# Kernel tuning notes

Measured on AMD Instinct MI355X. Metric: run time of the kernel, lower is better.

Reference implementation:

```python
import jax, jax.numpy as jnp
import numpy as np

N_NODES = 50000
N_EDGES = 800000
NODE_DIM = 64
EDGE_DIM = 32


def _glorot(key, shape):
    fan_in, fan_out = shape
    lim = (6.0 / (fan_in + fan_out)) ** 0.5
    return jax.random.uniform(key, shape, jnp.float32, -lim, lim)


def setup_inputs() -> dict:
    key = jax.random.key(0)
    ks = jax.random.split(key, 12)
    x = jax.random.normal(ks[0], (N_NODES, NODE_DIM), jnp.float32)
    edge_index = jax.random.randint(ks[1], (2, N_EDGES), 0, N_NODES, jnp.int64)
    edge_attr = jax.random.normal(ks[2], (N_EDGES, EDGE_DIM), jnp.float32)
    # edge_mlp: Linear(edge_dim + 2*node_dim -> node_dim), ReLU, Linear(node_dim -> node_dim)
    W1e = _glorot(ks[3], (EDGE_DIM + 2 * NODE_DIM, NODE_DIM))
    b1e = jnp.zeros((NODE_DIM,), jnp.float32)
    W2e = _glorot(ks[4], (NODE_DIM, NODE_DIM))
    b2e = jnp.zeros((NODE_DIM,), jnp.float32)
    # node_mlp: Linear(2*node_dim -> node_dim), ReLU, Linear(node_dim -> node_dim)
    W1n = _glorot(ks[5], (2 * NODE_DIM, NODE_DIM))
    b1n = jnp.zeros((NODE_DIM,), jnp.float32)
    W2n = _glorot(ks[6], (NODE_DIM, NODE_DIM))
    b2n = jnp.zeros((NODE_DIM,), jnp.float32)
    return {"x": x, "edge_index": edge_index, "edge_attr": edge_attr,
            "W1e": W1e, "b1e": b1e, "W2e": W2e, "b2e": b2e,
            "W1n": W1n, "b1n": b1n, "W2n": W2n, "b2n": b2n}


def reference(x, edge_index, edge_attr, W1e, b1e, W2e, b2e, W1n, b1n, W2n, b2n):
    row, col = edge_index[0], edge_index[1]
    # gather endpoint features: [E, node_dim] each
    edge_input = jnp.concatenate([x[row], x[col], edge_attr], axis=-1)  # [E, 2D+De]
    h = jax.nn.relu(edge_input @ W1e + b1e)
    edge_output = h @ W2e + b2e  # [E, D]
    # scatter-add into target nodes
    aggregated = jnp.zeros_like(x).at[col].add(edge_output)  # [N, D]
    node_input = jnp.concatenate([x, aggregated], axis=-1)  # [N, 2D]
    g = jax.nn.relu(node_input @ W1n + b1n)
    node_output = g @ W2n + b2n
    return jax.nn.relu(node_output + x)
```

## Files before the change

kernel.cpp:

```cpp
#include <hip/hip_runtime.h>

typedef float    f32x4 __attribute__((ext_vector_type(4)));
typedef short    s16x8 __attribute__((ext_vector_type(8)));
typedef unsigned u32x2 __attribute__((ext_vector_type(2)));

#define ND   64
#define DE   32
#define K1   160
#define K1P  168
#define K2P  72
#define KN   128
#define KNP  136

__device__ __forceinline__ ushort f2bf(float f) {
  unsigned u = __float_as_uint(f);
  return (ushort)((u + 0x7fffu + ((u >> 16) & 1u)) >> 16);
}
__device__ __forceinline__ float relu_f(float v) { return v > 0.f ? v : 0.f; }
__device__ __forceinline__ unsigned cvtpk(float lo, float hi) {
  unsigned r;
  asm("v_cvt_pk_bf16_f32 %0, %1, %2" : "=v"(r) : "v"(lo), "v"(hi));
  return r;
}

__launch_bounds__(256, 3)
__global__ void gc_edge(const float* __restrict__ x,
                        const int* __restrict__ eidx,
                        const float* __restrict__ eattr,
                        const float* __restrict__ W1e, const float* __restrict__ b1e,
                        ushort* __restrict__ hsum,
                        float* __restrict__ deg,
                        int E, int ngroups) {
  __shared__ ushort   w1t[ND][K1P];
  __shared__ ushort   strip[4][16][K1P];
  __shared__ unsigned hb[4][16][33];

  const int t    = threadIdx.x;
  const int lane = t & 63;
  const int w    = t >> 6;
  const int l15  = lane & 15;
  const int lhi  = lane >> 4;
  const int k8   = lhi * 8;

  for (int i = t; i < K1 * ND; i += 256) w1t[i & 63][i >> 6] = f2bf(W1e[i]);
  __syncthreads();

  float bias[4];
  #pragma unroll
  for (int n = 0; n < 4; ++n) bias[n] = b1e[n * 16 + l15];

  const int el   = lane >> 2;
  const int part = lane & 3;
  const int wid  = blockIdx.x * 4 + w;
  const int nw   = gridDim.x * 4;

  for (int g = wid; g < ngroups; g += nw) {
    const int e0 = g * 16;
    int myidx = 0;
    if (lane < 32)
      myidx = (lane < 16) ? eidx[e0 + lane] : eidx[E + e0 + (lane - 16)];

    const int rrow = __shfl(myidx, el);
    const int rcol = __shfl(myidx, 16 + el);
    const float* xr = x + (size_t)rrow * ND + part * 4;
    const float* xc = x + (size_t)rcol * ND + part * 4;
    const float* ap = eattr + ((size_t)e0 + (lane >> 3)) * DE + (lane & 7) * 4;

    f32x4 vr[4], vc[4], va[2];
    #pragma unroll
    for (int i = 0; i < 4; ++i) vr[i] = *(const f32x4*)(xr + i * 16);
    #pragma unroll
    for (int i = 0; i < 4; ++i) vc[i] = *(const f32x4*)(xc + i * 16);
    va[0] = *(const f32x4*)ap;
    va[1] = *(const f32x4*)(ap + 8 * DE);

    #pragma unroll
    for (int i = 0; i < 4; ++i) {
      u32x2 d = { cvtpk(vr[i].x, vr[i].y), cvtpk(vr[i].z, vr[i].w) };
      *(u32x2*)&strip[w][el][i * 16 + part * 4] = d;
    }
    #pragma unroll
    for (int i = 0; i < 4; ++i) {
      u32x2 d = { cvtpk(vc[i].x, vc[i].y), cvtpk(vc[i].z, vc[i].w) };
      *(u32x2*)&strip[w][el][64 + i * 16 + part * 4] = d;
    }
    #pragma unroll
    for (int i = 0; i < 2; ++i) {
      u32x2 d = { cvtpk(va[i].x, va[i].y), cvtpk(va[i].z, va[i].w) };
      *(u32x2*)&strip[w][(lane >> 3) + i * 8][128 + (lane & 7) * 4] = d;
    }
    asm volatile("s_waitcnt lgkmcnt(0)" ::: "memory");

    f32x4 acc[4] = {};
    #pragma unroll
    for (int ks = 0; ks < 5; ++ks) {
      s16x8 a = *(const s16x8*)&strip[w][l15][ks * 32 + k8];
      #pragma unroll
      for (int n = 0; n < 4; ++n) {
        s16x8 b = *(const s16x8*)&w1t[n * 16 + l15][ks * 32 + k8];
        acc[n] = __builtin_amdgcn_mfma_f32_16x16x32_bf16(a, b, acc[n], 0, 0, 0);
      }
    }

    if (lane >= 16 && lane < 32) atomicAdd(&deg[myidx], 1.0f);

    #pragma unroll
    for (int n = 0; n < 4; ++n) {
      #pragma unroll
      for (int j = 0; j < 4; ++j) {
        float r = relu_f(acc[n][j] + bias[n]);
        float p = __shfl_xor(r, 1);
        if (!(l15 & 1)) hb[w][lhi * 4 + j][(n * 16 + l15) >> 1] = cvtpk(r, p);
      }
    }
    asm volatile("s_waitcnt lgkmcnt(0)" ::: "memory");

    #pragma unroll
    for (int i = 0; i < 8; ++i) {
      int ee = (lane >> 4) + (i >> 1) * 4;
      int q  = (lane & 15) + (i & 1) * 16;
      int sc = __shfl(myidx, 16 + ee);
      uint64_t ad = (uint64_t)((unsigned*)hsum + (size_t)sc * 32 + q);
      unsigned data = hb[w][ee][q];
      asm volatile("global_atomic_pk_add_bf16 %0, %1, off" :: "v"(ad), "v"(data) : "memory");
    }
  }
}

__launch_bounds__(256, 2)
__global__ void gc_node(const float* __restrict__ x,
                        const ushort* __restrict__ hsum,
                        const float* __restrict__ deg,
                        const float* __restrict__ W2e, const float* __restrict__ b2e,
                        const float* __restrict__ W1n, const float* __restrict__ b1n,
                        const float* __restrict__ W2n, const float* __restrict__ b2n,
                        float* __restrict__ out, int N) {
  __shared__ ushort w2et[ND][K2P];
  __shared__ ushort w1nt[ND][KNP];
  __shared__ ushort w2nt[ND][K2P];
  __shared__ ushort in_lds[64][KNP];
  __shared__ ushort h_lds[64][K2P];

  const int t    = threadIdx.x;
  const int lane = t & 63;
  const int w    = t >> 6;
  const int l15  = lane & 15;
  const int lhi  = lane >> 4;
  const int k8   = lhi * 8;

  for (int i = t; i < 64 * ND; i += 256) w2et[i & 63][i >> 6] = f2bf(W2e[i]);
  for (int i = t; i < KN * ND; i += 256) w1nt[i & 63][i >> 6] = f2bf(W1n[i]);
  for (int i = t; i < 64 * ND; i += 256) w2nt[i & 63][i >> 6] = f2bf(W2n[i]);

  const int n0 = blockIdx.x * 64;
  #pragma unroll
  for (int i = 0; i < 4; ++i) {
    int chunk = t + i * 256;
    int r = chunk >> 4, p = chunk & 15;
    int node = n0 + r; if (node >= N) node = N - 1;
    f32x4 v = *(const f32x4*)(x + (size_t)node * ND + p * 4);
    unsigned* dst = (unsigned*)&in_lds[r][p * 4];
    dst[0] = cvtpk(v.x, v.y); dst[1] = cvtpk(v.z, v.w);
  }

  const int strip = w * 16;
  {
    int arow = strip + l15;
    int node = n0 + arow; if (node >= N) node = N - 1;
    const s16x8* ph = (const s16x8*)(hsum + (size_t)node * ND);
    s16x8 a0 = ph[lhi];
    s16x8 a1 = ph[4 + lhi];
    __syncthreads();
    f32x4 accg[4] = {};
    #pragma unroll
    for (int n = 0; n < 4; ++n) {
      s16x8 b0 = *(const s16x8*)&w2et[n * 16 + l15][k8];
      s16x8 b1 = *(const s16x8*)&w2et[n * 16 + l15][32 + k8];
      accg[n] = __builtin_amdgcn_mfma_f32_16x16x32_bf16(a0, b0, accg[n], 0, 0, 0);
      accg[n] = __builtin_amdgcn_mfma_f32_16x16x32_bf16(a1, b1, accg[n], 0, 0, 0);
    }
    #pragma unroll
    for (int n = 0; n < 4; ++n) {
      int d = n * 16 + l15;
      float b2 = b2e[d];
      #pragma unroll
      for (int j = 0; j < 4; ++j) {
        int r = strip + lhi * 4 + j;
        int node2 = n0 + r; if (node2 >= N) node2 = N - 1;
        float ag = accg[n][j] + deg[node2] * b2;
        in_lds[r][64 + d] = f2bf(ag);
      }
    }
  }
  __syncthreads();

  const int ar = strip + l15;
  f32x4 acc1[4] = {};
  #pragma unroll
  for (int ks = 0; ks < 4; ++ks) {
    s16x8 a = *(const s16x8*)&in_lds[ar][ks * 32 + k8];
    #pragma unroll
    for (int n = 0; n < 4; ++n) {
      s16x8 b = *(const s16x8*)&w1nt[n * 16 + l15][ks * 32 + k8];
      acc1[n] = __builtin_amdgcn_mfma_f32_16x16x32_bf16(a, b, acc1[n], 0, 0, 0);
    }
  }
  #pragma unroll
  for (int n = 0; n < 4; ++n) {
    int d = n * 16 + l15;
    float bias = b1n[d];
    #pragma unroll
    for (int j = 0; j < 4; ++j)
      h_lds[strip + lhi * 4 + j][d] = f2bf(relu_f(acc1[n][j] + bias));
  }
  __syncthreads();

  f32x4 acc2[4] = {};
  #pragma unroll
  for (int ks = 0; ks < 2; ++ks) {
    s16x8 a = *(const s16x8*)&h_lds[ar][ks * 32 + k8];
    #pragma unroll
    for (int n = 0; n < 4; ++n) {
      s16x8 b = *(const s16x8*)&w2nt[n * 16 + l15][ks * 32 + k8];
      acc2[n] = __builtin_amdgcn_mfma_f32_16x16x32_bf16(a, b, acc2[n], 0, 0, 0);
    }
  }
  #pragma unroll
  for (int n = 0; n < 4; ++n) {
    int d = n * 16 + l15;
    float bias = b2n[d];
    #pragma unroll
    for (int j = 0; j < 4; ++j) {
      int node = n0 + strip + lhi * 4 + j;
      if (node < N) {
        float xv = x[(size_t)node * ND + d];
        out[(size_t)node * ND + d] = relu_f(acc2[n][j] + bias + xv);
      }
    }
  }
}

extern "C" void kernel_launch(void* const* d_in, const int* in_sizes, int n_in,
                              void* d_out, int out_size, void* d_ws, size_t ws_size,
                              hipStream_t stream) {
  const float* x     = (const float*)d_in[0];
  const int*   eidx  = (const int*)d_in[1];
  const float* eattr = (const float*)d_in[2];
  const float* W1e   = (const float*)d_in[3];
  const float* b1e   = (const float*)d_in[4];
  const float* W2e   = (const float*)d_in[5];
  const float* b2e   = (const float*)d_in[6];
  const float* W1n   = (const float*)d_in[7];
  const float* b1n   = (const float*)d_in[8];
  const float* W2n   = (const float*)d_in[9];
  const float* b2n   = (const float*)d_in[10];
  float* out = (float*)d_out;

  const int N = in_sizes[0] / ND;
  const int E = in_sizes[1] / 2;
  const int ngroups = E / 16;

  ushort* hsum = (ushort*)d_ws;
  float*  degp = (float*)(hsum + (size_t)N * ND);

  hipMemsetAsync(d_ws, 0, (size_t)N * ND * 2 + (size_t)N * 4, stream);

  gc_edge<<<2048, 256, 0, stream>>>(x, eidx, eattr, W1e, b1e, hsum, degp, E, ngroups);

  int grid_n = (N + 63) / 64;
  gc_node<<<grid_n, 256, 0, stream>>>(x, hsum, degp, W2e, b2e, W1n, b1n, W2n, b2n, out, N);
}
```

Measured before the change: 167.7 us.

## Bucket edges by destination node to replace global atomics with LDS accumulation

Adds a counting-sort preprocessing pipeline (histogram, prefix scan, placement) that groups edges into 32-node buckets by destination, so each block handles one bucket. The destination node features come from an LDS window and the per-edge results accumulate in LDS with shared atomics before one bf16 store per node. This aims to remove the global bf16 scatter atomics and the repeated gathers of destination rows. In exchange it adds three extra launches, a single-block serial scan, an extra global pass over the edges with global atomics, and possible load imbalance across buckets. The old atomic path is kept as a fallback when the workspace is too small.

```diff
diff --git a/kernel.cpp b/kernel.cpp
--- a/kernel.cpp
+++ b/kernel.cpp
@@ -8,9 +8,13 @@
 #define DE   32
 #define K1   160
 #define K1P  168
+#define SP   104
+#define XWP  72
 #define K2P  72
 #define KN   128
 #define KNP  136
+#define BKT  32
+#define EMASK 0x1FFFFFF
 
 __device__ __forceinline__ ushort f2bf(float f) {
   unsigned u = __float_as_uint(f);
@@ -23,17 +27,66 @@
   return r;
 }
 
+__global__ void gc_hist(const int* __restrict__ eidx, float* __restrict__ deg, int E) {
+  int i = blockIdx.x * blockDim.x + threadIdx.x;
+  for (; i < E; i += gridDim.x * blockDim.x)
+    atomicAdd(&deg[eidx[E + i]], 1.0f);
+}
+
+__global__ void gc_prefix(const float* __restrict__ deg, int N, int NB,
+                          int* __restrict__ offset, int* __restrict__ cursor) {
+  __shared__ int cnt[2048];
+  const int t = threadIdx.x;
+  for (int b = t; b < NB; b += 256) {
+    int s = 0, base = b * BKT;
+    #pragma unroll
+    for (int j = 0; j < BKT; ++j) {
+      int node = base + j;
+      s += (node < N) ? (int)deg[node] : 0;
+    }
+    cnt[b] = s;
+  }
+  __syncthreads();
+  if (t < 64) {
+    int running = 0;
+    for (int base = 0; base < NB; base += 64) {
+      int b = base + t;
+      int v = (b < NB) ? cnt[b] : 0;
+      int incl = v;
+      #pragma unroll
+      for (int d = 1; d < 64; d <<= 1) {
+        int u = __shfl_up(incl, d);
+        if (t >= d) incl += u;
+      }
+      if (b < NB) { int ex = running + incl - v; offset[b] = ex; cursor[b] = ex; }
+      running += __shfl(incl, 63);
+    }
+    if (t == 0) offset[NB] = running;
+  }
+}
+
+__global__ void gc_place(const int* __restrict__ eidx, int* __restrict__ cursor,
+                         int2* __restrict__ recs, int E) {
+  int i = blockIdx.x * blockDim.x + threadIdx.x;
+  for (; i < E; i += gridDim.x * blockDim.x) {
+    int col = eidx[E + i];
+    int row = eidx[i];
+    int b = col >> 5;
+    int pos = atomicAdd(&cursor[b], 1);
+    recs[pos] = make_int2(row, ((col & 31) << 25) | i);
+  }
+}
+
 __launch_bounds__(256, 3)
-__global__ void gc_edge(const float* __restrict__ x,
-                        const int* __restrict__ eidx,
-                        const float* __restrict__ eattr,
-                        const float* __restrict__ W1e, const float* __restrict__ b1e,
-                        ushort* __restrict__ hsum,
-                        float* __restrict__ deg,
-                        int E, int ngroups) {
-  __shared__ ushort   w1t[ND][K1P];
-  __shared__ ushort   strip[4][16][K1P];
-  __shared__ unsigned hb[4][16][33];
+__global__ void gc_edge_b(const float* __restrict__ x,
+                          const float* __restrict__ eattr,
+                          const float* __restrict__ W1e, const float* __restrict__ b1e,
+                          const int2* __restrict__ recs, const int* __restrict__ offset,
+                          ushort* __restrict__ hsum, int N) {
+  __shared__ ushort w1t[ND][K1P];
+  __shared__ ushort strip[4][16][SP];
+  __shared__ ushort xwin[BKT][XWP];
+  __shared__ float  acc[BKT][ND];
 
   const int t    = threadIdx.x;
   const int lane = t & 63;
@@ -41,18 +94,138 @@
   const int l15  = lane & 15;
   const int lhi  = lane >> 4;
   const int k8   = lhi * 8;
+  const int bkt  = blockIdx.x;
+  const int node0 = bkt * BKT;
 
   for (int i = t; i < K1 * ND; i += 256) w1t[i & 63][i >> 6] = f2bf(W1e[i]);
+  #pragma unroll
+  for (int i = 0; i < 2; ++i) {
+    int c = t + i * 256;
+    int r = c >> 4, p = c & 15;
+    int node = node0 + r;
+    f32x4 v = {0.f, 0.f, 0.f, 0.f};
+    if (node < N) v = *(const f32x4*)(x + (size_t)node * ND + p * 4);
+    u32x2 d = { cvtpk(v.x, v.y), cvtpk(v.z, v.w) };
+    *(u32x2*)&xwin[r][p * 4] = d;
+  }
+  #pragma unroll
+  for (int i = 0; i < 8; ++i) {
+    int c = t + i * 256;
+    acc[c >> 6][c & 63] = 0.f;
+  }
   __syncthreads();
 
   float bias[4];
   #pragma unroll
   for (int n = 0; n < 4; ++n) bias[n] = b1e[n * 16 + l15];
 
-  const int el   = lane >> 2;
-  const int part = lane & 3;
-  const int wid  = blockIdx.x * 4 + w;
-  const int nw   = gridDim.x * 4;
+  const int start = offset[bkt], end = offset[bkt + 1];
+  const int nIter = (end - start + 63) >> 6;
+  const int el = lane >> 2, part = lane & 3;
+
+  for (int it = 0; it < nIter; ++it) {
+    const int eBase = start + it * 64 + w * 16;
+    int recx = 0, recy = 0;
+    if (lane < 16) {
+      int idx = eBase + lane;
+      if (idx >= end) idx = end - 1;
+      int2 r_ = recs[idx];
+      recx = r_.x; recy = r_.y;
+    }
+    const int rowv  = __shfl(recx, el);
+    const int eidA  = __shfl(recy, lane >> 3) & EMASK;
+    const int eidB  = __shfl(recy, 8 + (lane >> 3)) & EMASK;
+    const int myloc = __shfl(recy, l15) >> 25;
+
+    const float* xr = x + (size_t)rowv * ND + part * 4;
+    f32x4 vr[4];
+    #pragma unroll
+    for (int i = 0; i < 4; ++i) vr[i] = *(const f32x4*)(xr + i * 16);
+    f32x4 va0 = *(const f32x4*)(eattr + (size_t)eidA * DE + (lane & 7) * 4);
+    f32x4 va1 = *(const f32x4*)(eattr + (size_t)eidB * DE + (lane & 7) * 4);
+
+    #pragma unroll
+    for (int i = 0; i < 4; ++i) {
+      u32x2 d = { cvtpk(vr[i].x, vr[i].y), cvtpk(vr[i].z, vr[i].w) };
+      *(u32x2*)&strip[w][el][i * 16 + part * 4] = d;
+    }
+    { u32x2 d = { cvtpk(va0.x, va0.y), cvtpk(va0.z, va0.w) };
+      *(u32x2*)&strip[w][lane >> 3][64 + (lane & 7) * 4] = d; }
+    { u32x2 d = { cvtpk(va1.x, va1.y), cvtpk(va1.z, va1.w) };
+      *(u32x2*)&strip[w][8 + (lane >> 3)][64 + (lane & 7) * 4] = d; }
+    asm volatile("s_waitcnt lgkmcnt(0)" ::: "memory");
+
+    s16x8 a0 = *(const s16x8*)&strip[w][l15][k8];
+    s16x8 a1 = *(const s16x8*)&strip[w][l15][32 + k8];
+    s16x8 a2 = *(const s16x8*)&xwin[myloc][k8];
+    s16x8 a3 = *(const s16x8*)&xwin[myloc][32 + k8];
+    s16x8 a4 = *(const s16x8*)&strip[w][l15][64 + k8];
+
+    f32x4 accv[4] = {};
+    #pragma unroll
+    for (int n = 0; n < 4; ++n) {
+      const ushort* wr = &w1t[n * 16 + l15][0];
+      accv[n] = __builtin_amdgcn_mfma_f32_16x16x32_bf16(a0, *(const s16x8*)&wr[k8],        accv[n], 0, 0, 0);
+      accv[n] = __builtin_amdgcn_mfma_f32_16x16x32_bf16(a1, *(const s16x8*)&wr[32 + k8],   accv[n], 0, 0, 0);
+      accv[n] = __builtin_amdgcn_mfma_f32_16x16x32_bf16(a2, *(const s16x8*)&wr[64 + k8],   accv[n], 0, 0, 0);
+      accv[n] = __builtin_amdgcn_mfma_f32_16x16x32_bf16(a3, *(const s16x8*)&wr[96 + k8],   accv[n], 0, 0, 0);
+      accv[n] = __builtin_amdgcn_mfma_f32_16x16x32_bf16(a4, *(const s16x8*)&wr[128 + k8],  accv[n], 0, 0, 0);
+    }
+
+    #pragma unroll
+    for (int j = 0; j < 4; ++j) {
+      const int  locj  = __shfl(recy, lhi * 4 + j) >> 25;
+      const bool valid = (eBase + lhi * 4 + j) < end;
+      if (valid) {
+        #pragma unroll
+        for (int n = 0; n < 4; ++n)
+          atomicAdd(&acc[locj][n * 16 + l15], relu_f(accv[n][j] + bias[n]));
+      }
+    }
+  }
+  __syncthreads();
+
+  #pragma unroll
+  for (int i = 0; i < 2; ++i) {
+    int c = t + i * 256;
+    int r = c >> 4, p = (c & 15) * 4;
+    int node = node0 + r;
+    if (node < N) {
+      f32x4 v = *(const f32x4*)&acc[r][p];
+      u32x2 d = { cvtpk(v.x, v.y), cvtpk(v.z, v.w) };
+      *(u32x2*)&hsum[(size_t)node * ND + p] = d;
+    }
+  }
+}
+
+__launch_bounds__(256, 3)
+__global__ void gc_edge_atomic(const float* __restrict__ x,
+                               const int* __restrict__ eidx,
+                               const float* __restrict__ eattr,
+                               const float* __restrict__ W1e, const float* __restrict__ b1e,
+                               ushort* __restrict__ hsum, float* __restrict__ deg,
+                               int E, int ngroups) {
+  __shared__ ushort   w1t[ND][K1P];
+  __shared__ ushort   strip[4][16][K1P];
+  __shared__ unsigned hb[4][16][33];
+
+  const int t    = threadIdx.x;
+  const int lane = t & 63;
+  const int w    = t >> 6;
+  const int l15  = lane & 15;
+  const int lhi  = lane >> 4;
+  const int k8   = lhi * 8;
+
+  for (int i = t; i < K1 * ND; i += 256) w1t[i & 63][i >> 6] = f2bf(W1e[i]);
+  __syncthreads();
+
+  float bias[4];
+  #pragma unroll
+  for (int n = 0; n < 4; ++n) bias[n] = b1e[n * 16 + l15];
+
+  const int el = lane >> 2, part = lane & 3;
+  const int wid = blockIdx.x * 4 + w;
+  const int nw  = gridDim.x * 4;
 
   for (int g = wid; g < ngroups; g += nw) {
     const int e0 = g * 16;
@@ -256,17 +429,30 @@
   const float* b2n   = (const float*)d_in[10];
   float* out = (float*)d_out;
 
-  const int N = in_sizes[0] / ND;
-  const int E = in_sizes[1] / 2;
-  const int ngroups = E / 16;
-
-  ushort* hsum = (ushort*)d_ws;
-  float*  degp = (float*)(hsum + (size_t)N * ND);
-
-  hipMemsetAsync(d_ws, 0, (size_t)N * ND * 2 + (size_t)N * 4, stream);
-
-  gc_edge<<<2048, 256, 0, stream>>>(x, eidx, eattr, W1e, b1e, hsum, degp, E, ngroups);
+  const int N  = in_sizes[0] / ND;
+  const int E  = in_sizes[1] / 2;
+  const int NB = (N + BKT - 1) / BKT;
+
+  char* ws = (char*)d_ws;
+  ushort* hsum   = (ushort*)ws;
+  float*  deg    = (float*)(ws + (size_t)N * ND * 2);
+  size_t  off    = (size_t)N * ND * 2 + (size_t)N * 4;
+  int2*   recs   = (int2*)(ws + off);
+  int*    offset = (int*)(ws + off + (size_t)E * 8);
+  int*    cursor = offset + (NB + 1);
+  size_t  need   = off + (size_t)E * 8 + (size_t)(2 * NB + 1) * 4;
+
+  if (ws_size >= need) {
+    hipMemsetAsync(deg, 0, (size_t)N * 4, stream);
+    gc_hist<<<1024, 256, 0, stream>>>(eidx, deg, E);
+    gc_prefix<<<1, 256, 0, stream>>>(deg, N, NB, offset, cursor);
+    gc_place<<<1024, 256, 0, stream>>>(eidx, cursor, recs, E);
+    gc_edge_b<<<NB, 256, 0, stream>>>(x, eattr, W1e, b1e, recs, offset, hsum, N);
+  } else {
+    hipMemsetAsync(d_ws, 0, (size_t)N * ND * 2 + (size_t)N * 4, stream);
+    gc_edge_atomic<<<2048, 256, 0, stream>>>(x, eidx, eattr, W1e, b1e, hsum, deg, E, E / 16);
+  }
 
   int grid_n = (N + 63) / 64;
-  gc_node<<<grid_n, 256, 0, stream>>>(x, hsum, degp, W2e, b2e, W1n, b1n, W2n, b2n, out, N);
-}
+  gc_node<<<grid_n, 256, 0, stream>>>(x, hsum, deg, W2e, b2e, W1n, b1n, W2n, b2n, out, N);
+}
```

Result: slower. 566.6 us (+237.9%).

## Replace atomic scatter-add with CSR sort and per-node gather aggregation

Applied to the files above, without the earlier changes.

The edge kernel now writes each edge's hidden activation to a per-edge bf16 buffer instead of atomically adding into node sums. A single-block prefix scan over the degree counts and an atomic placement pass then build a CSR list of edges grouped by target node. A gather kernel sums each node's incoming edges without atomics. W1 fragments are also preloaded into registers. This trades the contended bf16 atomics for extra kernels, a serial single-block scan, and a large per-edge intermediate buffer. If the workspace is too small, the code falls back to the old atomic path.

```diff
diff --git a/kernel.cpp b/kernel.cpp
--- a/kernel.cpp
+++ b/kernel.cpp
@@ -3,6 +3,7 @@
 typedef float    f32x4 __attribute__((ext_vector_type(4)));
 typedef short    s16x8 __attribute__((ext_vector_type(8)));
 typedef unsigned u32x2 __attribute__((ext_vector_type(2)));
+typedef unsigned u32x4 __attribute__((ext_vector_type(4)));
 
 #define ND   64
 #define DE   32
@@ -16,6 +17,7 @@
   unsigned u = __float_as_uint(f);
   return (ushort)((u + 0x7fffu + ((u >> 16) & 1u)) >> 16);
 }
+__device__ __forceinline__ float bf2f(unsigned u) { return __uint_as_float(u << 16); }
 __device__ __forceinline__ float relu_f(float v) { return v > 0.f ? v : 0.f; }
 __device__ __forceinline__ unsigned cvtpk(float lo, float hi) {
   unsigned r;
@@ -24,16 +26,16 @@
 }
 
 __launch_bounds__(256, 3)
-__global__ void gc_edge(const float* __restrict__ x,
-                        const int* __restrict__ eidx,
-                        const float* __restrict__ eattr,
-                        const float* __restrict__ W1e, const float* __restrict__ b1e,
-                        ushort* __restrict__ hsum,
-                        float* __restrict__ deg,
-                        int E, int ngroups) {
+__global__ void gc_edge_h(const float* __restrict__ x,
+                          const int* __restrict__ eidx,
+                          const float* __restrict__ eattr,
+                          const float* __restrict__ W1e, const float* __restrict__ b1e,
+                          ushort* __restrict__ hbuf,
+                          float* __restrict__ deg,
+                          int E, int ngroups) {
   __shared__ ushort   w1t[ND][K1P];
   __shared__ ushort   strip[4][16][K1P];
-  __shared__ unsigned hb[4][16][33];
+  __shared__ unsigned hb[4][16][36];
 
   const int t    = threadIdx.x;
   const int lane = t & 63;
@@ -45,14 +47,193 @@
   for (int i = t; i < K1 * ND; i += 256) w1t[i & 63][i >> 6] = f2bf(W1e[i]);
   __syncthreads();
 
+  s16x8 bf[4][5];
+  #pragma unroll
+  for (int n = 0; n < 4; ++n)
+    #pragma unroll
+    for (int ks = 0; ks < 5; ++ks)
+      bf[n][ks] = *(const s16x8*)&w1t[n * 16 + l15][ks * 32 + k8];
+
   float bias[4];
   #pragma unroll
   for (int n = 0; n < 4; ++n) bias[n] = b1e[n * 16 + l15];
 
-  const int el   = lane >> 2;
-  const int part = lane & 3;
-  const int wid  = blockIdx.x * 4 + w;
-  const int nw   = gridDim.x * 4;
+  const int el = lane >> 2, part = lane & 3;
+  const int wid = blockIdx.x * 4 + w;
+  const int nw  = gridDim.x * 4;
+
+  for (int g = wid; g < ngroups; g += nw) {
+    const int e0 = g * 16;
+    int myidx = 0;
+    if (lane < 32)
+      myidx = (lane < 16) ? eidx[e0 + lane] : eidx[E + e0 + (lane - 16)];
+
+    const int rrow = __shfl(myidx, el);
+    const int rcol = __shfl(myidx, 16 + el);
+    const float* xr = x + (size_t)rrow * ND + part * 4;
+    const float* xc = x + (size_t)rcol * ND + part * 4;
+    const float* ap = eattr + ((size_t)e0 + (lane >> 3)) * DE + (lane & 7) * 4;
+
+    f32x4 vr[4], vc[4], va[2];
+    #pragma unroll
+    for (int i = 0; i < 4; ++i) vr[i] = *(const f32x4*)(xr + i * 16);
+    #pragma unroll
+    for (int i = 0; i < 4; ++i) vc[i] = *(const f32x4*)(xc + i * 16);
+    va[0] = *(const f32x4*)ap;
+    va[1] = *(const f32x4*)(ap + 8 * DE);
+
+    #pragma unroll
+    for (int i = 0; i < 4; ++i) {
+      u32x2 d = { cvtpk(vr[i].x, vr[i].y), cvtpk(vr[i].z, vr[i].w) };
+      *(u32x2*)&strip[w][el][i * 16 + part * 4] = d;
+    }
+    #pragma unroll
+    for (int i = 0; i < 4; ++i) {
+      u32x2 d = { cvtpk(vc[i].x, vc[i].y), cvtpk(vc[i].z, vc[i].w) };
+      *(u32x2*)&strip[w][el][64 + i * 16 + part * 4] = d;
+    }
+    #pragma unroll
+    for (int i = 0; i < 2; ++i) {
+      u32x2 d = { cvtpk(va[i].x, va[i].y), cvtpk(va[i].z, va[i].w) };
+      *(u32x2*)&strip[w][(lane >> 3) + i * 8][128 + (lane & 7) * 4] = d;
+    }
+    asm volatile("s_waitcnt lgkmcnt(0)" ::: "memory");
+
+    f32x4 acc[4] = {};
+    #pragma unroll
+    for (int ks = 0; ks < 5; ++ks) {
+      s16x8 a = *(const s16x8*)&strip[w][l15][ks * 32 + k8];
+      #pragma unroll
+      for (int n = 0; n < 4; ++n)
+        acc[n] = __builtin_amdgcn_mfma_f32_16x16x32_bf16(a, bf[n][ks], acc[n], 0, 0, 0);
+    }
+
+    if (lane >= 16 && lane < 32) atomicAdd(&deg[myidx], 1.0f);
+
+    #pragma unroll
+    for (int n = 0; n < 4; ++n) {
+      #pragma unroll
+      for (int j = 0; j < 4; ++j) {
+        float r = relu_f(acc[n][j] + bias[n]);
+        float p = __shfl_xor(r, 1);
+        if (!(l15 & 1)) hb[w][lhi * 4 + j][(n * 16 + l15) >> 1] = cvtpk(r, p);
+      }
+    }
+    asm volatile("s_waitcnt lgkmcnt(0)" ::: "memory");
+
+    unsigned* hrow = (unsigned*)hbuf + (size_t)(e0 + (lane >> 2)) * 32 + (lane & 3) * 4;
+    u32x4 d0 = *(const u32x4*)&hb[w][lane >> 2][(lane & 3) * 4];
+    u32x4 d1 = *(const u32x4*)&hb[w][lane >> 2][(lane & 3) * 4 + 16];
+    *(u32x4*)hrow = d0;
+    *(u32x4*)(hrow + 16) = d1;
+  }
+}
+
+__global__ void gc_prefix(const float* __restrict__ deg, int N,
+                          int* __restrict__ offset, int* __restrict__ cursor) {
+  __shared__ int wt[16], we[16];
+  __shared__ int srun, ctot;
+  const int t = threadIdx.x, lane = t & 63, w = t >> 6;
+  if (t == 0) srun = 0;
+  __syncthreads();
+  for (int base = 0; base < N; base += 1024) {
+    int i = base + t;
+    int v = (i < N) ? (int)deg[i] : 0;
+    int incl = v;
+    #pragma unroll
+    for (int d = 1; d < 64; d <<= 1) {
+      int u = __shfl_up(incl, d);
+      if (lane >= d) incl += u;
+    }
+    if (lane == 63) wt[w] = incl;
+    __syncthreads();
+    if (t == 0) {
+      int run = 0;
+      #pragma unroll
+      for (int k = 0; k < 16; ++k) { we[k] = run; run += wt[k]; }
+      ctot = run;
+    }
+    __syncthreads();
+    if (i < N) {
+      int ex = srun + we[w] + incl - v;
+      offset[i] = ex; cursor[i] = ex;
+    }
+    __syncthreads();
+    if (t == 0) srun += ctot;
+    __syncthreads();
+  }
+  if (t == 0) offset[N] = srun;
+}
+
+__global__ void gc_place(const int* __restrict__ eidx, int* __restrict__ cursor,
+                         int* __restrict__ recs, int E) {
+  int i = blockIdx.x * blockDim.x + threadIdx.x;
+  for (; i < E; i += gridDim.x * blockDim.x) {
+    int col = eidx[E + i];
+    int pos = atomicAdd(&cursor[col], 1);
+    recs[pos] = i;
+  }
+}
+
+__launch_bounds__(256, 8)
+__global__ void gc_agg(const ushort* __restrict__ hbuf,
+                       const int* __restrict__ recs,
+                       const int* __restrict__ offset,
+                       ushort* __restrict__ hsum, int N) {
+  const int t = threadIdx.x, lane = t & 63, w = t >> 6;
+  const int v = blockIdx.x * 4 + w;
+  if (v >= N) return;
+  const int g = lane >> 4, l15 = lane & 15;
+  const int start = offset[v], end = offset[v + 1];
+
+  float a0 = 0.f, a1 = 0.f, a2 = 0.f, a3 = 0.f;
+  for (int c = start; c < end; c += 4) {
+    int idx = c + g;
+    if (idx < end) {
+      int eid = recs[idx];
+      u32x2 d = *(const u32x2*)(hbuf + (size_t)eid * ND + l15 * 4);
+      a0 += bf2f(d.x & 0xffffu); a1 += bf2f(d.x >> 16);
+      a2 += bf2f(d.y & 0xffffu); a3 += bf2f(d.y >> 16);
+    }
+  }
+  a0 += __shfl_xor(a0, 16); a1 += __shfl_xor(a1, 16);
+  a2 += __shfl_xor(a2, 16); a3 += __shfl_xor(a3, 16);
+  a0 += __shfl_xor(a0, 32); a1 += __shfl_xor(a1, 32);
+  a2 += __shfl_xor(a2, 32); a3 += __shfl_xor(a3, 32);
+  if (lane < 16) {
+    u32x2 o = { cvtpk(a0, a1), cvtpk(a2, a3) };
+    *(u32x2*)&hsum[(size_t)v * ND + l15 * 4] = o;
+  }
+}
+
+__launch_bounds__(256, 3)
+__global__ void gc_edge_atomic(const float* __restrict__ x,
+                               const int* __restrict__ eidx,
+                               const float* __restrict__ eattr,
+                               const float* __restrict__ W1e, const float* __restrict__ b1e,
+                               ushort* __restrict__ hsum, float* __restrict__ deg,
+                               int E, int ngroups) {
+  __shared__ ushort   w1t[ND][K1P];
+  __shared__ ushort   strip[4][16][K1P];
+  __shared__ unsigned hb[4][16][33];
+
+  const int t    = threadIdx.x;
+  const int lane = t & 63;
+  const int w    = t >> 6;
+  const int l15  = lane & 15;
+  const int lhi  = lane >> 4;
+  const int k8   = lhi * 8;
+
+  for (int i = t; i < K1 * ND; i += 256) w1t[i & 63][i >> 6] = f2bf(W1e[i]);
+  __syncthreads();
+
+  float bias[4];
+  #pragma unroll
+  for (int n = 0; n < 4; ++n) bias[n] = b1e[n * 16 + l15];
+
+  const int el = lane >> 2, part = lane & 3;
+  const int wid = blockIdx.x * 4 + w;
+  const int nw  = gridDim.x * 4;
 
   for (int g = wid; g < ngroups; g += nw) {
     const int e0 = g * 16;
@@ -258,15 +439,29 @@
 
   const int N = in_sizes[0] / ND;
   const int E = in_sizes[1] / 2;
-  const int ngroups = E / 16;
-
-  ushort* hsum = (ushort*)d_ws;
-  float*  degp = (float*)(hsum + (size_t)N * ND);
-
-  hipMemsetAsync(d_ws, 0, (size_t)N * ND * 2 + (size_t)N * 4, stream);
-
-  gc_edge<<<2048, 256, 0, stream>>>(x, eidx, eattr, W1e, b1e, hsum, degp, E, ngroups);
-
-  int grid_n = (N + 63) / 64;
-  gc_node<<<grid_n, 256, 0, stream>>>(x, hsum, degp, W2e, b2e, W1n, b1n, W2n, b2n, out, N);
-}
+
+  char* ws = (char*)d_ws;
+  ushort* hbuf   = (ushort*)ws;
+  ushort* hsum   = (ushort*)(ws + (size_t)E * ND * 2);
+  float*  deg    = (float*)(ws + (size_t)E * ND * 2 + (size_t)N * ND * 2);
+  int*    offset = (int*)((char*)deg + (size_t)N * 4);
+  int*    cursor = offset + (N + 1);
+  int*    recs   = cursor + N;
+  size_t need = (size_t)E * ND * 2 + (size_t)N * ND * 2 + (size_t)N * 4
+              + (size_t)(2 * N + 1) * 4 + (size_t)E * 4;
+
+  if (ws_size >= need) {
+    hipMemsetAsync(deg, 0, (size_t)N * 4, stream);
+    gc_edge_h<<<2048, 256, 0, stream>>>(x, eidx, eattr, W1e, b1e, hbuf, deg, E, E / 16);
+    gc_prefix<<<1, 1024, 0, stream>>>(deg, N, offset, cursor);
+    gc_place<<<1024, 256, 0, stream>>>(eidx, cursor, recs, E);
+    gc_agg<<<(N + 3) / 4, 256, 0, stream>>>(hbuf, recs, offset, hsum, N);
+    gc_node<<<(N + 63) / 64, 256, 0, stream>>>(x, hsum, deg, W2e, b2e, W1n, b1n, W2n, b2n, out, N);
+  } else {
+    ushort* hsum_fb = (ushort*)ws;
+    float*  deg_fb  = (float*)(ws + (size_t)N * ND * 2);
+    hipMemsetAsync(ws, 0, (size_t)N * ND * 2 + (size_t)N * 4, stream);
+    gc_edge_atomic<<<2048, 256, 0, stream>>>(x, eidx, eattr, W1e, b1e, hsum_fb, deg_fb, E, E / 16);
+    gc_node<<<(N + 63) / 64, 256, 0, stream>>>(x, hsum_fb, deg_fb, W2e, b2e, W1n, b1n, W2n, b2n, out, N);
+  }
+}
```

Result: slower. 253.0 us (+50.9%).

## Precompute per-node projections of x through W1e and gather them per edge

Applied to the files above, without the earlier changes.

The first edge-MLP layer is split algebraically into x[row]@W1a + x[col]@W1b + attr@W1c. A new kernel computes both node projections once per node into a bf16 PQ buffer. The edge kernel then gathers 64-dim bf16 projections instead of 128 fp32 features, runs only the 32-wide attribute MFMA, adds the three parts and applies ReLU before the atomic scatter. This cuts per-edge gather bytes and MFMA work, at the cost of an extra kernel, an extra workspace buffer, and bf16 rounding of the intermediate projections.

```diff
diff --git a/kernel.cpp b/kernel.cpp
--- a/kernel.cpp
+++ b/kernel.cpp
@@ -3,14 +3,14 @@
 typedef float    f32x4 __attribute__((ext_vector_type(4)));
 typedef short    s16x8 __attribute__((ext_vector_type(8)));
 typedef unsigned u32x2 __attribute__((ext_vector_type(2)));
+typedef unsigned u32x4 __attribute__((ext_vector_type(4)));
 
 #define ND   64
 #define DE   32
-#define K1   160
-#define K1P  168
-#define K2P  72
 #define KN   128
 #define KNP  136
+#define K2P  72
+#define WBP  40
 
 __device__ __forceinline__ ushort f2bf(float f) {
   unsigned u = __float_as_uint(f);
@@ -22,37 +22,101 @@
   asm("v_cvt_pk_bf16_f32 %0, %1, %2" : "=v"(r) : "v"(lo), "v"(hi));
   return r;
 }
-
-__launch_bounds__(256, 3)
-__global__ void gc_edge(const float* __restrict__ x,
-                        const int* __restrict__ eidx,
-                        const float* __restrict__ eattr,
-                        const float* __restrict__ W1e, const float* __restrict__ b1e,
-                        ushort* __restrict__ hsum,
-                        float* __restrict__ deg,
-                        int E, int ngroups) {
-  __shared__ ushort   w1t[ND][K1P];
-  __shared__ ushort   strip[4][16][K1P];
-  __shared__ unsigned hb[4][16][33];
-
-  const int t    = threadIdx.x;
-  const int lane = t & 63;
-  const int w    = t >> 6;
-  const int l15  = lane & 15;
-  const int lhi  = lane >> 4;
-  const int k8   = lhi * 8;
-
-  for (int i = t; i < K1 * ND; i += 256) w1t[i & 63][i >> 6] = f2bf(W1e[i]);
+__device__ __forceinline__ float bflo(unsigned u) { return __uint_as_float(u << 16); }
+__device__ __forceinline__ float bfhi(unsigned u) { return __uint_as_float(u & 0xffff0000u); }
+
+__launch_bounds__(256, 2)
+__global__ void gc_pq(const float* __restrict__ x,
+                      const float* __restrict__ W1e,
+                      unsigned* __restrict__ PQ,
+                      int N) {
+  __shared__ ushort xl[64][K2P];
+  __shared__ ushort wtA[ND][K2P];
+  __shared__ ushort wtB[ND][K2P];
+
+  const int t = threadIdx.x, lane = t & 63, w = t >> 6;
+  const int l15 = lane & 15, lhi = lane >> 4, k8 = lhi * 8;
+
+  for (int i = t; i < ND * ND; i += 256) {
+    wtA[i & 63][i >> 6] = f2bf(W1e[i]);
+    wtB[i & 63][i >> 6] = f2bf(W1e[(size_t)ND * ND + i]);
+  }
+  const int n0 = blockIdx.x * 64;
+  #pragma unroll
+  for (int i = 0; i < 4; ++i) {
+    int chunk = t + i * 256;
+    int r = chunk >> 4, p = chunk & 15;
+    int node = n0 + r; if (node >= N) node = N - 1;
+    f32x4 v = *(const f32x4*)(x + (size_t)node * ND + p * 4);
+    unsigned* dst = (unsigned*)&xl[r][p * 4];
+    dst[0] = cvtpk(v.x, v.y); dst[1] = cvtpk(v.z, v.w);
+  }
   __syncthreads();
 
+  const int strip = w * 16;
+  const int ar = strip + l15;
+  s16x8 a0 = *(const s16x8*)&xl[ar][k8];
+  s16x8 a1 = *(const s16x8*)&xl[ar][32 + k8];
+
+  f32x4 accP[4] = {}, accQ[4] = {};
+  #pragma unroll
+  for (int n = 0; n < 4; ++n) {
+    s16x8 bA0 = *(const s16x8*)&wtA[n * 16 + l15][k8];
+    s16x8 bA1 = *(const s16x8*)&wtA[n * 16 + l15][32 + k8];
+    s16x8 bB0 = *(const s16x8*)&wtB[n * 16 + l15][k8];
+    s16x8 bB1 = *(const s16x8*)&wtB[n * 16 + l15][32 + k8];
+    accP[n] = __builtin_amdgcn_mfma_f32_16x16x32_bf16(a0, bA0, accP[n], 0, 0, 0);
+    accP[n] = __builtin_amdgcn_mfma_f32_16x16x32_bf16(a1, bA1, accP[n], 0, 0, 0);
+    accQ[n] = __builtin_amdgcn_mfma_f32_16x16x32_bf16(a0, bB0, accQ[n], 0, 0, 0);
+    accQ[n] = __builtin_amdgcn_mfma_f32_16x16x32_bf16(a1, bB1, accQ[n], 0, 0, 0);
+  }
+  #pragma unroll
+  for (int n = 0; n < 4; ++n) {
+    #pragma unroll
+    for (int j = 0; j < 4; ++j) {
+      int node = n0 + strip + lhi * 4 + j;
+      float rP = accP[n][j];  float pP = __shfl_xor(rP, 1);
+      float rQ = accQ[n][j];  float pQ = __shfl_xor(rQ, 1);
+      if (!(l15 & 1) && node < N) {
+        unsigned dw = (unsigned)(n * 16 + l15) >> 1;
+        PQ[(size_t)node * 64 + dw]      = cvtpk(rP, pP);
+        PQ[(size_t)node * 64 + 32 + dw] = cvtpk(rQ, pQ);
+      }
+    }
+  }
+}
+
+__launch_bounds__(256, 4)
+__global__ void gc_edge_pq(const int* __restrict__ eidx,
+                           const float* __restrict__ eattr,
+                           const float* __restrict__ W1e, const float* __restrict__ b1e,
+                           const unsigned* __restrict__ PQ,
+                           unsigned* __restrict__ hsum,
+                           float* __restrict__ deg,
+                           int E, int ngroups) {
+  __shared__ ushort   w1bt[ND][WBP];
+  __shared__ unsigned hb[4][16][32];
+
+  const int t = threadIdx.x, lane = t & 63, w = t >> 6;
+  const int l15 = lane & 15, lhi = lane >> 4, k8 = lhi * 8;
+
+  for (int i = t; i < DE * ND; i += 256)
+    w1bt[i & 63][i >> 6] = f2bf(W1e[(size_t)KN * ND + i]);
+  __syncthreads();
+
+  s16x8 bfr[4];
+  #pragma unroll
+  for (int n = 0; n < 4; ++n) bfr[n] = *(const s16x8*)&w1bt[n * 16 + l15][k8];
+
   float bias[4];
   #pragma unroll
   for (int n = 0; n < 4; ++n) bias[n] = b1e[n * 16 + l15];
 
-  const int el   = lane >> 2;
-  const int part = lane & 3;
-  const int wid  = blockIdx.x * 4 + w;
-  const int nw   = gridDim.x * 4;
+  const int e8   = lane >> 3;
+  const int part = lane & 7;
+
+  const int wid = blockIdx.x * 4 + w;
+  const int nw  = gridDim.x * 4;
 
   for (int g = wid; g < ngroups; g += nw) {
     const int e0 = g * 16;
@@ -60,47 +124,27 @@
     if (lane < 32)
       myidx = (lane < 16) ? eidx[e0 + lane] : eidx[E + e0 + (lane - 16)];
 
-    const int rrow = __shfl(myidx, el);
-    const int rcol = __shfl(myidx, 16 + el);
-    const float* xr = x + (size_t)rrow * ND + part * 4;
-    const float* xc = x + (size_t)rcol * ND + part * 4;
-    const float* ap = eattr + ((size_t)e0 + (lane >> 3)) * DE + (lane & 7) * 4;
-
-    f32x4 vr[4], vc[4], va[2];
-    #pragma unroll
-    for (int i = 0; i < 4; ++i) vr[i] = *(const f32x4*)(xr + i * 16);
-    #pragma unroll
-    for (int i = 0; i < 4; ++i) vc[i] = *(const f32x4*)(xc + i * 16);
-    va[0] = *(const f32x4*)ap;
-    va[1] = *(const f32x4*)(ap + 8 * DE);
-
-    #pragma unroll
-    for (int i = 0; i < 4; ++i) {
-      u32x2 d = { cvtpk(vr[i].x, vr[i].y), cvtpk(vr[i].z, vr[i].w) };
-      *(u32x2*)&strip[w][el][i * 16 + part * 4] = d;
-    }
-    #pragma unroll
-    for (int i = 0; i < 4; ++i) {
-      u32x2 d = { cvtpk(vc[i].x, vc[i].y), cvtpk(vc[i].z, vc[i].w) };
-      *(u32x2*)&strip[w][el][64 + i * 16 + part * 4] = d;
-    }
-    #pragma unroll
-    for (int i = 0; i < 2; ++i) {
-      u32x2 d = { cvtpk(va[i].x, va[i].y), cvtpk(va[i].z, va[i].w) };
-      *(u32x2*)&strip[w][(lane >> 3) + i * 8][128 + (lane & 7) * 4] = d;
-    }
-    asm volatile("s_waitcnt lgkmcnt(0)" ::: "memory");
+    const int r0 = __shfl(myidx, e8);
+    const int r1 = __shfl(myidx, 8 + e8);
+    const int c0 = __shfl(myidx, 16 + e8);
+    const int c1 = __shfl(myidx, 24 + e8);
+
+    u32x4 P0 = *(const u32x4*)(PQ + (size_t)r0 * 64 + part * 4);
+    u32x4 P1 = *(const u32x4*)(PQ + (size_t)r1 * 64 + part * 4);
+    u32x4 Q0 = *(const u32x4*)(PQ + (size_t)c0 * 64 + 32 + part * 4);
+    u32x4 Q1 = *(const u32x4*)(PQ + (size_t)c1 * 64 + 32 + part * 4);
+
+    const float* ap = eattr + ((size_t)e0 + l15) * DE + k8;
+    f32x4 alo = __builtin_nontemporal_load((const f32x4*)ap);
+    f32x4 ahi = __builtin_nontemporal_load((const f32x4*)(ap + 4));
+    union { unsigned u[4]; s16x8 v; } af;
+    af.u[0] = cvtpk(alo.x, alo.y); af.u[1] = cvtpk(alo.z, alo.w);
+    af.u[2] = cvtpk(ahi.x, ahi.y); af.u[3] = cvtpk(ahi.z, ahi.w);
 
     f32x4 acc[4] = {};
     #pragma unroll
-    for (int ks = 0; ks < 5; ++ks) {
-      s16x8 a = *(const s16x8*)&strip[w][l15][ks * 32 + k8];
-      #pragma unroll
-      for (int n = 0; n < 4; ++n) {
-        s16x8 b = *(const s16x8*)&w1t[n * 16 + l15][ks * 32 + k8];
-        acc[n] = __builtin_amdgcn_mfma_f32_16x16x32_bf16(a, b, acc[n], 0, 0, 0);
-      }
-    }
+    for (int n = 0; n < 4; ++n)
+      acc[n] = __builtin_amdgcn_mfma_f32_16x16x32_bf16(af.v, bfr[n], acc[n], 0, 0, 0);
 
     if (lane >= 16 && lane < 32) atomicAdd(&deg[myidx], 1.0f);
 
@@ -108,21 +152,33 @@
     for (int n = 0; n < 4; ++n) {
       #pragma unroll
       for (int j = 0; j < 4; ++j) {
-        float r = relu_f(acc[n][j] + bias[n]);
+        float r = acc[n][j] + bias[n];
         float p = __shfl_xor(r, 1);
         if (!(l15 & 1)) hb[w][lhi * 4 + j][(n * 16 + l15) >> 1] = cvtpk(r, p);
       }
     }
     asm volatile("s_waitcnt lgkmcnt(0)" ::: "memory");
 
-    #pragma unroll
-    for (int i = 0; i < 8; ++i) {
-      int ee = (lane >> 4) + (i >> 1) * 4;
-      int q  = (lane & 15) + (i & 1) * 16;
-      int sc = __shfl(myidx, 16 + ee);
-      uint64_t ad = (uint64_t)((unsigned*)hsum + (size_t)sc * 32 + q);
-      unsigned data = hb[w][ee][q];
-      asm volatile("global_atomic_pk_add_bf16 %0, %1, off" :: "v"(ad), "v"(data) : "memory");
+    u32x4 R0 = *(const u32x4*)&hb[w][e8][part * 4];
+    u32x4 R1 = *(const u32x4*)&hb[w][8 + e8][part * 4];
+
+    unsigned* h0 = hsum + (size_t)c0 * 32 + part * 4;
+    unsigned* h1 = hsum + (size_t)c1 * 32 + part * 4;
+    #pragma unroll
+    for (int k = 0; k < 4; ++k) {
+      float slo = relu_f(bflo(P0[k]) + bflo(Q0[k]) + bflo(R0[k]));
+      float shi = relu_f(bfhi(P0[k]) + bfhi(Q0[k]) + bfhi(R0[k]));
+      unsigned dw = cvtpk(slo, shi);
+      asm volatile("global_atomic_pk_add_bf16 %0, %1, off"
+                   :: "v"((uint64_t)(h0 + k)), "v"(dw) : "memory");
+    }
+    #pragma unroll
+    for (int k = 0; k < 4; ++k) {
+      float slo = relu_f(bflo(P1[k]) + bflo(Q1[k]) + bflo(R1[k]));
+      float shi = relu_f(bfhi(P1[k]) + bfhi(Q1[k]) + bfhi(R1[k]));
+      unsigned dw = cvtpk(slo, shi);
+      asm volatile("global_atomic_pk_add_bf16 %0, %1, off"
+                   :: "v"((uint64_t)(h1 + k)), "v"(dw) : "memory");
     }
   }
 }
@@ -258,15 +314,17 @@
 
   const int N = in_sizes[0] / ND;
   const int E = in_sizes[1] / 2;
-  const int ngroups = E / 16;
-
-  ushort* hsum = (ushort*)d_ws;
-  float*  degp = (float*)(hsum + (size_t)N * ND);
-
-  hipMemsetAsync(d_ws, 0, (size_t)N * ND * 2 + (size_t)N * 4, stream);
-
-  gc_edge<<<2048, 256, 0, stream>>>(x, eidx, eattr, W1e, b1e, hsum, degp, E, ngroups);
-
-  int grid_n = (N + 63) / 64;
-  gc_node<<<grid_n, 256, 0, stream>>>(x, hsum, degp, W2e, b2e, W1n, b1n, W2n, b2n, out, N);
-}
+
+  char* ws = (char*)d_ws;
+  unsigned* hsum = (unsigned*)ws;
+  float*    deg  = (float*)(ws + (size_t)N * ND * 2);
+  unsigned* PQ   = (unsigned*)(ws + (size_t)N * ND * 2 + (size_t)N * 4);
+
+  hipMemsetAsync(ws, 0, (size_t)N * ND * 2 + (size_t)N * 4, stream);
+
+  gc_pq<<<(N + 63) / 64, 256, 0, stream>>>(x, W1e, PQ, N);
+  gc_edge_pq<<<2048, 256, 0, stream>>>(eidx, eattr, W1e, b1e, PQ,
+                                       hsum, deg, E, E / 16);
+  gc_node<<<(N + 63) / 64, 256, 0, stream>>>(x, (const ushort*)hsum, deg,
+                                             W2e, b2e, W1n, b1n, W2n, b2n, out, N);
+}
```

Result: slower. 412.9 us (+146.2%).
